# Kernel optimization log

Hardware: AMD Instinct MI355X
Metric: run time of the kernel (lower is better)

Reference implementation:

```python
import jax, jax.numpy as jnp
import numpy as np

N, E, CIN, COUT = 100000, 1600000, 64, 128
EPS = 1e-5  # torch BatchNorm default


def setup_inputs() -> dict:
    key = jax.random.key(0)
    ks = jax.random.split(key, 16)
    s = 0.1
    x = jax.random.normal(ks[0], (N, CIN), jnp.float32)
    src = jax.random.randint(ks[1], (E,), 0, N, dtype=jnp.int32)
    dst = jax.random.randint(ks[2], (E,), 0, N, dtype=jnp.int32)
    edge_index = jnp.stack([src, dst])  # [2, E]
    return {
        "x": x,
        "edge_index": edge_index,
        # conv0: GraphConv(CIN -> COUT)
        "W_root0": jax.random.normal(ks[3], (COUT, CIN), jnp.float32) * s,
        "W_nbr0": jax.random.normal(ks[4], (COUT, CIN), jnp.float32) * s,
        "b0": jnp.zeros((COUT,), jnp.float32),
        # bn0
        "g0": jnp.ones((COUT,), jnp.float32),
        "be0": jnp.zeros((COUT,), jnp.float32),
        # conv1: GraphConv(COUT -> COUT)
        "W_root1": jax.random.normal(ks[5], (COUT, COUT), jnp.float32) * s,
        "W_nbr1": jax.random.normal(ks[6], (COUT, COUT), jnp.float32) * s,
        "b1": jnp.zeros((COUT,), jnp.float32),
        # bn1
        "g1": jnp.ones((COUT,), jnp.float32),
        "be1": jnp.zeros((COUT,), jnp.float32),
        # residual 1x1 conv (Conv1d(CIN, COUT, 1))
        "Wlin": jax.random.normal(ks[7], (COUT, CIN), jnp.float32) * s,
        "blin": jnp.zeros((COUT,), jnp.float32),
    }


def graph_conv(x, src, dst, W_root, W_nbr, b):
    # PyG GraphConv: out_i = W_root x_i + W_nbr * sum_{j: (j->i) in E} x_j + b
    agg = jax.ops.segment_sum(x[src], dst, num_segments=N)  # scatter-add over edges
    return x @ W_root.T + agg @ W_nbr.T + b


def batch_norm(x, gamma, beta):
    # training-mode BatchNorm over the node dimension (biased variance)
    mu = jnp.mean(x, axis=0)
    var = jnp.mean(jnp.square(x - mu), axis=0)
    return (x - mu) * jax.lax.rsqrt(var + EPS) * gamma + beta


def reference(x, edge_index, W_root0, W_nbr0, b0, g0, be0,
              W_root1, W_nbr1, b1, g1, be1, Wlin, blin):
    src, dst = edge_index[0], edge_index[1]
    y = batch_norm(graph_conv(x, src, dst, W_root0, W_nbr0, b0), g0, be0)
    y = jax.nn.relu(y)
    y = batch_norm(graph_conv(y, src, dst, W_root1, W_nbr1, b1), g1, be1)
    out = y + (x @ Wlin.T + blin)  # 1x1 Conv1d residual projection
    return jax.nn.relu(out)
```

## Files before the change

### kernel.cpp

```cpp
#include <hip/hip_runtime.h>
#include <stdint.h>


#define CIN 64
#define COUT 128
#define BN_EPS 1e-5f
#define CURPAD 32
#define PCPAD 32
#define SPAD 32
#define PSH 8
#define PNODES (1 << PSH)
#define MAXP 512

typedef unsigned short u16;
typedef short short8 __attribute__((ext_vector_type(8)));
typedef float f32x4 __attribute__((ext_vector_type(4)));

__device__ __forceinline__ float bf2f(u16 u) {
    union { unsigned int i; float f; } v; v.i = ((unsigned int)u) << 16; return v.f;
}
__device__ __forceinline__ u16 f2bf(float f) {
    union { float f; unsigned int i; } v; v.f = f;
    unsigned int r = v.i + 0x7fffu + ((v.i >> 16) & 1u);
    return (u16)(r >> 16);
}
__device__ __forceinline__ float lo16(unsigned int w) { return bf2f((u16)(w & 0xffffu)); }
__device__ __forceinline__ float hi16(unsigned int w) { return bf2f((u16)(w >> 16)); }

template<bool BF> __device__ __forceinline__ float ldf(const void* p, long i) {
    if (BF) return bf2f(((const u16*)p)[i]);
    return ((const float*)p)[i];
}
template<bool BF> __device__ __forceinline__ short8 ld8(const void* p, long i) {
    if (BF) return *(const short8*)((const u16*)p + i);
    const float* f = (const float*)p + i;
    short8 r;
#pragma unroll
    for (int j = 0; j < 8; ++j) r[j] = (short)f2bf(f[j]);
    return r;
}

__global__ void k_detect(const unsigned int* __restrict__ x, int* __restrict__ flag) {
    int lane = threadIdx.x;
    int cnt = 0;
#pragma unroll
    for (int i = 0; i < 8; ++i) {
        unsigned int w = x[lane * 8 + i];
        unsigned int e0 = (w >> 7) & 0xFFu, e1 = (w >> 23) & 0xFFu;
        cnt += (e0 >= 0x60u && e0 <= 0x8Eu);
        cnt += (e1 >= 0x60u && e1 <= 0x8Eu);
    }
    for (int o = 32; o; o >>= 1) cnt += __shfl_down(cnt, o);
    if (lane == 0) *flag = (cnt > 850) ? 1 : 0;
}

__global__ __launch_bounds__(256) void k_phist(const int* __restrict__ dst,
                                               int* __restrict__ pcount, int E, int np) {
    __shared__ int h[MAXP];
    for (int i = threadIdx.x; i < np; i += 256) h[i] = 0;
    __syncthreads();
    int stride = gridDim.x * 256;
    for (int e = blockIdx.x * 256 + threadIdx.x; e < E; e += stride)
        atomicAdd(&h[dst[e] >> PSH], 1);
    __syncthreads();
    for (int i = threadIdx.x; i < np; i += 256)
        if (h[i]) atomicAdd(&pcount[i * PCPAD], h[i]);
}

__global__ void k_pscan(const int* __restrict__ pcount, int* __restrict__ pstart,
                        int* __restrict__ pcursor, int np, int E) {
    __shared__ int s[MAXP];
    int t = threadIdx.x;
    int v = (t < np) ? pcount[t * PCPAD] : 0;
    s[t] = v; __syncthreads();
    for (int o = 1; o < MAXP; o <<= 1) {
        int u = (t >= o) ? s[t - o] : 0;
        __syncthreads(); s[t] += u; __syncthreads();
    }
    if (t < np) {
        int ex = s[t] - v;
        pstart[t] = ex;
        pcursor[t * CURPAD] = ex;
    }
    if (t == 0) pstart[np] = E;
}

__global__ __launch_bounds__(256) void k_pfill(const int* __restrict__ src,
        const int* __restrict__ dst, int* __restrict__ pcursor,
        unsigned int* __restrict__ barr, int E, int np) {
    __shared__ int cnt[MAXP], gb[MAXP], loc[MAXP];
    int tid = threadIdx.x;
    int base = blockIdx.x * 4096;
    for (int i = tid; i < np; i += 256) { cnt[i] = 0; loc[i] = 0; }
    __syncthreads();
    int pk[16]; unsigned int rec[16];
#pragma unroll
    for (int k = 0; k < 16; ++k) {
        int e = base + k * 256 + tid;
        if (e < E) {
            int d = dst[e];
            pk[k] = d >> PSH;
            rec[k] = ((unsigned int)(d & (PNODES - 1)) << 20) | (unsigned int)src[e];
            atomicAdd(&cnt[pk[k]], 1);
        } else pk[k] = -1;
    }
    __syncthreads();
    for (int i = tid; i < np; i += 256)
        if (cnt[i]) gb[i] = atomicAdd(&pcursor[i * CURPAD], cnt[i]);
    __syncthreads();
#pragma unroll
    for (int k = 0; k < 16; ++k) {
        if (pk[k] >= 0) {
            int off = atomicAdd(&loc[pk[k]], 1);
            barr[gb[pk[k]] + off] = rec[k];
        }
    }
}

__global__ __launch_bounds__(256) void k_psort(const unsigned int* __restrict__ barr,
        const int* __restrict__ pstart, int* __restrict__ csr,
        int* __restrict__ row_start, int n, int np, int E) {
    __shared__ int hist[PNODES], curs[PNODES], tsum[256];
    int tid = threadIdx.x;
    int p = blockIdx.x;
    int e0 = pstart[p], e1 = pstart[p + 1];
    int node0 = p << PSH;
    hist[tid] = 0;
    __syncthreads();
    for (int t = e0 + tid; t < e1; t += 256)
        atomicAdd(&hist[barr[t] >> 20], 1);
    __syncthreads();
    int v = hist[tid];
    tsum[tid] = v; __syncthreads();
    for (int o = 1; o < 256; o <<= 1) {
        int u = (tid >= o) ? tsum[tid - o] : 0;
        __syncthreads(); tsum[tid] += u; __syncthreads();
    }
    int ex = tsum[tid] - v;
    curs[tid] = ex;
    int nd = node0 + tid;
    if (nd < n) row_start[nd] = e0 + ex;
    if (p == np - 1 && tid == 0) row_start[n] = E;
    __syncthreads();
    for (int t = e0 + tid; t < e1; t += 256) {
        unsigned int rec = barr[t];
        int pos = atomicAdd(&curs[rec >> 20], 1);
        csr[e0 + pos] = (int)(rec & 0xFFFFF);
    }
}

template<bool BF>
__device__ __forceinline__ void agg0_impl(const void* x, const int* rs, const int* csr,
                                          u16* agg, int n) {
    int i = blockIdx.x * 4 + (threadIdx.x >> 6);
    if (i >= n) return;
    int lane = threadIdx.x & 63;
    int slot = lane >> 4, cp = lane & 15;
    int b = rs[i], e = rs[i + 1];
    if (BF) {
        const unsigned int* x32 = (const unsigned int*)x;
        float acc[4] = {0.f, 0.f, 0.f, 0.f};
        int t = b + slot;
        for (; t + 12 < e; t += 16) {
            int j0 = csr[t], j1 = csr[t + 4], j2 = csr[t + 8], j3 = csr[t + 12];
            uint2 w0 = *((const uint2*)(x32 + (long)j0 * 32) + cp);
            uint2 w1 = *((const uint2*)(x32 + (long)j1 * 32) + cp);
            uint2 w2 = *((const uint2*)(x32 + (long)j2 * 32) + cp);
            uint2 w3 = *((const uint2*)(x32 + (long)j3 * 32) + cp);
            acc[0] += lo16(w0.x) + lo16(w1.x); acc[1] += hi16(w0.x) + hi16(w1.x);
            acc[2] += lo16(w0.y) + lo16(w1.y); acc[3] += hi16(w0.y) + hi16(w1.y);
            acc[0] += lo16(w2.x) + lo16(w3.x); acc[1] += hi16(w2.x) + hi16(w3.x);
            acc[2] += lo16(w2.y) + lo16(w3.y); acc[3] += hi16(w2.y) + hi16(w3.y);
        }
        for (; t < e; t += 4) {
            int j0 = csr[t];
            uint2 w0 = *((const uint2*)(x32 + (long)j0 * 32) + cp);
            acc[0] += lo16(w0.x); acc[1] += hi16(w0.x);
            acc[2] += lo16(w0.y); acc[3] += hi16(w0.y);
        }
#pragma unroll
        for (int k = 0; k < 4; ++k) {
            acc[k] += __shfl_xor(acc[k], 16);
            acc[k] += __shfl_xor(acc[k], 32);
        }
        if (slot == 0) {
            uint2 o;
            o.x = (unsigned int)f2bf(acc[0]) | ((unsigned int)f2bf(acc[1]) << 16);
            o.y = (unsigned int)f2bf(acc[2]) | ((unsigned int)f2bf(acc[3]) << 16);
            *((uint2*)((unsigned int*)agg + (long)i * 32) + cp) = o;
        }
    } else {
        float acc[4] = {0.f, 0.f, 0.f, 0.f};
        int t = b + slot;
        for (; t + 12 < e; t += 16) {
            int j0 = csr[t], j1 = csr[t + 4], j2 = csr[t + 8], j3 = csr[t + 12];
            float4 w0 = *((const float4*)((const float*)x + (long)j0 * 64) + cp);
            float4 w1 = *((const float4*)((const float*)x + (long)j1 * 64) + cp);
            float4 w2 = *((const float4*)((const float*)x + (long)j2 * 64) + cp);
            float4 w3 = *((const float4*)((const float*)x + (long)j3 * 64) + cp);
            acc[0] += (w0.x + w1.x) + (w2.x + w3.x);
            acc[1] += (w0.y + w1.y) + (w2.y + w3.y);
            acc[2] += (w0.z + w1.z) + (w2.z + w3.z);
            acc[3] += (w0.w + w1.w) + (w2.w + w3.w);
        }
        for (; t < e; t += 4) {
            int j0 = csr[t];
            float4 w0 = *((const float4*)((const float*)x + (long)j0 * 64) + cp);
            acc[0] += w0.x; acc[1] += w0.y; acc[2] += w0.z; acc[3] += w0.w;
        }
#pragma unroll
        for (int k = 0; k < 4; ++k) {
            acc[k] += __shfl_xor(acc[k], 16);
            acc[k] += __shfl_xor(acc[k], 32);
        }
        if (slot == 0) {
            uint2 o;
            o.x = (unsigned int)f2bf(acc[0]) | ((unsigned int)f2bf(acc[1]) << 16);
            o.y = (unsigned int)f2bf(acc[2]) | ((unsigned int)f2bf(acc[3]) << 16);
            *((uint2*)((unsigned int*)agg + (long)i * 32) + cp) = o;
        }
    }
}

__global__ __launch_bounds__(256) void k_agg0(const int* __restrict__ flag,
        const void* x, const int* __restrict__ rs, const int* __restrict__ csr,
        u16* __restrict__ agg, int n) {
    if (*flag) agg0_impl<true >(x, rs, csr, agg, n);
    else       agg0_impl<false>(x, rs, csr, agg, n);
}

__global__ __launch_bounds__(256) void k_y0p(unsigned int* __restrict__ y0,
        const float* __restrict__ sc, const float* __restrict__ sh, long nq) {
    long idx = (long)blockIdx.x * 256 + threadIdx.x;
    int colq = threadIdx.x & 15;
    float s8[8], h8[8];
#pragma unroll
    for (int j = 0; j < 8; ++j) { s8[j] = sc[colq * 8 + j]; h8[j] = sh[colq * 8 + j]; }
    long stride = (long)gridDim.x * 256;
    uint4* p = (uint4*)y0;
    for (; idx < nq; idx += stride) {
        uint4 w = p[idx];
        unsigned int r[4] = {w.x, w.y, w.z, w.w};
        uint4 o;
        unsigned int* po = (unsigned int*)&o;
#pragma unroll
        for (int d = 0; d < 4; ++d) {
            float a = fmaxf(lo16(r[d]) * s8[2 * d]     + h8[2 * d],     0.f);
            float b = fmaxf(hi16(r[d]) * s8[2 * d + 1] + h8[2 * d + 1], 0.f);
            po[d] = (unsigned int)f2bf(a) | ((unsigned int)f2bf(b) << 16);
        }
        p[idx] = o;
    }
}

__global__ __launch_bounds__(256) void k_agg1(const u16* __restrict__ y0p,
        const int* __restrict__ rs, const int* __restrict__ csr,
        u16* __restrict__ agg, int n) {
    int i = blockIdx.x * 4 + (threadIdx.x >> 6);
    if (i >= n) return;
    int lane = threadIdx.x & 63;
    int slot = lane >> 4, cp = lane & 15;
    const unsigned int* y32 = (const unsigned int*)y0p;
    int b = rs[i], e = rs[i + 1];
    float acc[8] = {0.f, 0.f, 0.f, 0.f, 0.f, 0.f, 0.f, 0.f};
    int t = b + slot;
    for (; t + 12 < e; t += 16) {
        int j0 = csr[t], j1 = csr[t + 4], j2 = csr[t + 8], j3 = csr[t + 12];
        uint4 w0 = *((const uint4*)(y32 + (long)j0 * 64) + cp);
        uint4 w1 = *((const uint4*)(y32 + (long)j1 * 64) + cp);
        uint4 w2 = *((const uint4*)(y32 + (long)j2 * 64) + cp);
        uint4 w3 = *((const uint4*)(y32 + (long)j3 * 64) + cp);
        acc[0] += lo16(w0.x) + lo16(w1.x); acc[1] += hi16(w0.x) + hi16(w1.x);
        acc[2] += lo16(w0.y) + lo16(w1.y); acc[3] += hi16(w0.y) + hi16(w1.y);
        acc[4] += lo16(w0.z) + lo16(w1.z); acc[5] += hi16(w0.z) + hi16(w1.z);
        acc[6] += lo16(w0.w) + lo16(w1.w); acc[7] += hi16(w0.w) + hi16(w1.w);
        acc[0] += lo16(w2.x) + lo16(w3.x); acc[1] += hi16(w2.x) + hi16(w3.x);
        acc[2] += lo16(w2.y) + lo16(w3.y); acc[3] += hi16(w2.y) + hi16(w3.y);
        acc[4] += lo16(w2.z) + lo16(w3.z); acc[5] += hi16(w2.z) + hi16(w3.z);
        acc[6] += lo16(w2.w) + lo16(w3.w); acc[7] += hi16(w2.w) + hi16(w3.w);
    }
    for (; t < e; t += 4) {
        int j0 = csr[t];
        uint4 w0 = *((const uint4*)(y32 + (long)j0 * 64) + cp);
        acc[0] += lo16(w0.x); acc[1] += hi16(w0.x);
        acc[2] += lo16(w0.y); acc[3] += hi16(w0.y);
        acc[4] += lo16(w0.z); acc[5] += hi16(w0.z);
        acc[6] += lo16(w0.w); acc[7] += hi16(w0.w);
    }
#pragma unroll
    for (int k = 0; k < 8; ++k) {
        acc[k] += __shfl_xor(acc[k], 16);
        acc[k] += __shfl_xor(acc[k], 32);
    }
    if (slot == 0) {
        uint4 o;
        o.x = (unsigned int)f2bf(acc[0]) | ((unsigned int)f2bf(acc[1]) << 16);
        o.y = (unsigned int)f2bf(acc[2]) | ((unsigned int)f2bf(acc[3]) << 16);
        o.z = (unsigned int)f2bf(acc[4]) | ((unsigned int)f2bf(acc[5]) << 16);
        o.w = (unsigned int)f2bf(acc[6]) | ((unsigned int)f2bf(acc[7]) << 16);
        *((uint4*)((unsigned int*)agg + (long)i * 64) + cp) = o;
    }
}

template<bool BF>
__device__ __forceinline__ void gemm0_impl(const void* x, const u16* agg,
                                           const void* Wr, const void* Wn,
                                           u16* y0, float* sumP, float* sqP,
                                           int n, int nch, u16* lds) {
    const int ST = 130;
    int tid = threadIdx.x;
    int wave = tid >> 6, lane = tid & 63, lr = lane & 15, q = lane >> 4;

    short8 wf[2][4];
#pragma unroll
    for (int i = 0; i < 2; ++i) {
        int c = (2 * wave + i) * 16 + lr;
#pragma unroll
        for (int ks = 0; ks < 4; ++ks) {
            const void* W = (ks < 2) ? Wr : Wn;
            wf[i][ks] = ld8<BF>(W, (long)c * CIN + (ks & 1) * 32 + q * 8);
        }
    }

    const int rowb = tid >> 3, wb = tid & 7;
    const int rowf = tid >> 4, wfc = tid & 15;
    short8 rbx[2]; float4 rfx[4]; short8 rag[2];

    auto regload = [&](long chunk0) {
        if (BF) {
#pragma unroll
            for (int i = 0; i < 2; ++i) {
                long rg = chunk0 + rowb + i * 32; if (rg > n - 1) rg = n - 1;
                rbx[i] = *(const short8*)((const u16*)x + rg * CIN + wb * 8);
            }
        } else {
#pragma unroll
            for (int i = 0; i < 4; ++i) {
                long rg = chunk0 + rowf + i * 16; if (rg > n - 1) rg = n - 1;
                rfx[i] = *(const float4*)((const float*)x + rg * CIN + wfc * 4);
            }
        }
#pragma unroll
        for (int i = 0; i < 2; ++i) {
            long rg = chunk0 + rowb + i * 32; if (rg > n - 1) rg = n - 1;
            rag[i] = *(const short8*)(agg + rg * CIN + wb * 8);
        }
    };

    float st[2] = {0.f, 0.f}, sq[2] = {0.f, 0.f};
    int ch = blockIdx.x;
    if (ch < nch) regload((long)ch * 64);
    for (; ch < nch; ch += gridDim.x) {
        long chunk0 = (long)ch * 64;
        __syncthreads();
        if (BF) {
#pragma unroll
            for (int i = 0; i < 2; ++i)
                *(short8*)(lds + (rowb + i * 32) * ST + wb * 8) = rbx[i];
        } else {
#pragma unroll
            for (int i = 0; i < 4; ++i) {
                u16* d = lds + (rowf + i * 16) * ST + wfc * 4;
                d[0] = f2bf(rfx[i].x); d[1] = f2bf(rfx[i].y);
                d[2] = f2bf(rfx[i].z); d[3] = f2bf(rfx[i].w);
            }
        }
#pragma unroll
        for (int i = 0; i < 2; ++i)
            *(short8*)(lds + (rowb + i * 32) * ST + 64 + wb * 8) = rag[i];
        __syncthreads();
        long nxt = (long)ch + gridDim.x;
        if (nxt < nch) regload(nxt * 64);

#pragma unroll
        for (int t = 0; t < 4; ++t) {
            short8 a[4];
#pragma unroll
            for (int ks = 0; ks < 4; ++ks)
                a[ks] = *(const short8*)(lds + (t * 16 + lr) * ST + ks * 32 + q * 8);
#pragma unroll
            for (int i = 0; i < 2; ++i) {
                f32x4 acc = {0.f, 0.f, 0.f, 0.f};
#pragma unroll
                for (int ks = 0; ks < 4; ++ks)
                    acc = __builtin_amdgcn_mfma_f32_16x16x32_bf16(a[ks], wf[i][ks], acc, 0, 0, 0);
                int c = (2 * wave + i) * 16 + lr;
#pragma unroll
                for (int r = 0; r < 4; ++r) {
                    long row = chunk0 + t * 16 + q * 4 + r;
                    if (row < n) {
                        y0[row * COUT + c] = f2bf(acc[r]);
                        st[i] += acc[r]; sq[i] += acc[r] * acc[r];
                    }
                }
            }
        }
    }
#pragma unroll
    for (int i = 0; i < 2; ++i) {
        st[i] += __shfl_xor(st[i], 16); st[i] += __shfl_xor(st[i], 32);
        sq[i] += __shfl_xor(sq[i], 16); sq[i] += __shfl_xor(sq[i], 32);
    }
    if (q == 0) {
#pragma unroll
        for (int i = 0; i < 2; ++i) {
            int c = (2 * wave + i) * 16 + lr;
            atomicAdd(&sumP[c * SPAD], st[i]);
            atomicAdd(&sqP[c * SPAD], sq[i]);
        }
    }
}

__global__ __launch_bounds__(256) void k_gemm0(const int* __restrict__ flag,
        const void* x, const u16* __restrict__ agg, const void* Wr, const void* Wn,
        u16* __restrict__ y0, float* __restrict__ sumP, float* __restrict__ sqP,
        int n, int nch) {
    __shared__ u16 lds[64 * 130];
    if (*flag) gemm0_impl<true >(x, agg, Wr, Wn, y0, sumP, sqP, n, nch, lds);
    else       gemm0_impl<false>(x, agg, Wr, Wn, y0, sumP, sqP, n, nch, lds);
}

template<bool BF>
__device__ __forceinline__ void gemm1_impl(const u16* y0p, const u16* agg,
                                           const void* Wr, const void* Wn,
                                           u16* y1, float* sumP, float* sqP,
                                           int n, int nch, u16* lds) {
    const int ST = 258;
    int tid = threadIdx.x;
    int wave = tid >> 6, lane = tid & 63, lr = lane & 15, q = lane >> 4;
    int c = wave * 16 + lr;

    short8 wf[8];
#pragma unroll
    for (int ks = 0; ks < 8; ++ks) {
        const void* W = (ks < 4) ? Wr : Wn;
        wf[ks] = ld8<BF>(W, (long)c * COUT + (ks & 3) * 32 + q * 8);
    }

    const int rowy = tid >> 4, wy = tid & 15;
    short8 ry[2], rag[2];
    auto regload = [&](long chunk0) {
#pragma unroll
        for (int i = 0; i < 2; ++i) {
            long rg = chunk0 + rowy + i * 32; if (rg > n - 1) rg = n - 1;
            ry[i]  = *(const short8*)(y0p + rg * COUT + wy * 8);
            rag[i] = *(const short8*)(agg + rg * COUT + wy * 8);
        }
    };

    float st = 0.f, sq = 0.f;
    int ch = blockIdx.x;
    if (ch < nch) regload((long)ch * 64);
    for (; ch < nch; ch += gridDim.x) {
        long chunk0 = (long)ch * 64;
        __syncthreads();
#pragma unroll
        for (int i = 0; i < 2; ++i) {
            *(short8*)(lds + (rowy + i * 32) * ST + wy * 8) = ry[i];
            *(short8*)(lds + (rowy + i * 32) * ST + 128 + wy * 8) = rag[i];
        }
        __syncthreads();
        long nxt = (long)ch + gridDim.x;
        if (nxt < nch) regload(nxt * 64);

#pragma unroll
        for (int t = 0; t < 4; ++t) {
            short8 a[8];
#pragma unroll
            for (int ks = 0; ks < 8; ++ks)
                a[ks] = *(const short8*)(lds + (t * 16 + lr) * ST + ks * 32 + q * 8);
            f32x4 acc = {0.f, 0.f, 0.f, 0.f};
#pragma unroll
            for (int ks = 0; ks < 8; ++ks)
                acc = __builtin_amdgcn_mfma_f32_16x16x32_bf16(a[ks], wf[ks], acc, 0, 0, 0);
#pragma unroll
            for (int r = 0; r < 4; ++r) {
                long row = chunk0 + t * 16 + q * 4 + r;
                if (row < n) {
                    y1[row * COUT + c] = f2bf(acc[r]);
                    st += acc[r]; sq += acc[r] * acc[r];
                }
            }
        }
    }
    st += __shfl_xor(st, 16); st += __shfl_xor(st, 32);
    sq += __shfl_xor(sq, 16); sq += __shfl_xor(sq, 32);
    if (q == 0) {
        atomicAdd(&sumP[c * SPAD], st);
        atomicAdd(&sqP[c * SPAD], sq);
    }
}

__global__ __launch_bounds__(512) void k_gemm1(const int* __restrict__ flag,
        const u16* __restrict__ y0p, const u16* __restrict__ agg,
        const void* Wr, const void* Wn,
        u16* y1_bf , u16* y1_ws,
        float* __restrict__ sumP, float* __restrict__ sqP, int n, int nch) {
    __shared__ u16 lds[64 * 258];
    u16* y1 = *flag ? y1_bf : y1_ws;
    if (*flag) gemm1_impl<true >(y0p, agg, Wr, Wn, y1, sumP, sqP, n, nch, lds);
    else       gemm1_impl<false>(y0p, agg, Wr, Wn, y1, sumP, sqP, n, nch, lds);
}

__global__ void k_bnfin(const int* __restrict__ flag,
                        const float* __restrict__ sumP, const float* __restrict__ sqP,
                        const void* g, const void* be,
                        float* __restrict__ scale, float* __restrict__ shift, int n) {
    int c = threadIdx.x;
    bool bf = (*flag != 0);
    float inv = 1.f / (float)n;
    float mu = sumP[c * SPAD] * inv;
    float var = fmaxf(sqP[c * SPAD] * inv - mu * mu, 0.f);
    float gv = bf ? bf2f(((const u16*)g)[c]) : ((const float*)g)[c];
    float bv = bf ? bf2f(((const u16*)be)[c]) : ((const float*)be)[c];
    float sc = gv * rsqrtf(var + BN_EPS);
    scale[c] = sc;
    shift[c] = bv - mu * sc;
}

template<bool BF>
__device__ __forceinline__ void final_impl(const void* x, const u16* y1,
                                           const void* Wlin, const void* blin,
                                           const float* sc, const float* sh,
                                           void* out, int n, int nch, u16* lds) {
    const int ST = 194;
    int tid = threadIdx.x;
    int wave = tid >> 6, lane = tid & 63, lr = lane & 15, q = lane >> 4;

    short8 wf[2][2];
    float blc[2], scc[2], shc[2];
#pragma unroll
    for (int i = 0; i < 2; ++i) {
        int c = (2 * wave + i) * 16 + lr;
#pragma unroll
        for (int ks = 0; ks < 2; ++ks)
            wf[i][ks] = ld8<BF>(Wlin, (long)c * CIN + ks * 32 + q * 8);
        blc[i] = ldf<BF>(blin, c);
        scc[i] = sc[c]; shc[i] = sh[c];
    }

    const int rowb = tid >> 3, wb = tid & 7;
    const int rowf = tid >> 4, wfc = tid & 15;
    const int rowy = tid >> 4, wy = tid & 15;
    short8 rbx[2]; float4 rfx[4]; short8 ry[4];

    auto regload = [&](long chunk0) {
        if (BF) {
#pragma unroll
            for (int i = 0; i < 2; ++i) {
                long rg = chunk0 + rowb + i * 32; if (rg > n - 1) rg = n - 1;
                rbx[i] = *(const short8*)((const u16*)x + rg * CIN + wb * 8);
            }
        } else {
#pragma unroll
            for (int i = 0; i < 4; ++i) {
                long rg = chunk0 + rowf + i * 16; if (rg > n - 1) rg = n - 1;
                rfx[i] = *(const float4*)((const float*)x + rg * CIN + wfc * 4);
            }
        }
#pragma unroll
        for (int i = 0; i < 4; ++i) {
            long rg = chunk0 + rowy + i * 16; if (rg > n - 1) rg = n - 1;
            ry[i] = *(const short8*)(y1 + rg * COUT + wy * 8);
        }
    };

    int ch = blockIdx.x;
    if (ch < nch) regload((long)ch * 64);
    for (; ch < nch; ch += gridDim.x) {
        long chunk0 = (long)ch * 64;
        __syncthreads();
        if (BF) {
#pragma unroll
            for (int i = 0; i < 2; ++i)
                *(short8*)(lds + (rowb + i * 32) * ST + wb * 8) = rbx[i];
        } else {
#pragma unroll
            for (int i = 0; i < 4; ++i) {
                u16* d = lds + (rowf + i * 16) * ST + wfc * 4;
                d[0] = f2bf(rfx[i].x); d[1] = f2bf(rfx[i].y);
                d[2] = f2bf(rfx[i].z); d[3] = f2bf(rfx[i].w);
            }
        }
#pragma unroll
        for (int i = 0; i < 4; ++i)
            *(short8*)(lds + (rowy + i * 16) * ST + 64 + wy * 8) = ry[i];
        __syncthreads();
        long nxt = (long)ch + gridDim.x;
        if (nxt < nch) regload(nxt * 64);

#pragma unroll
        for (int t = 0; t < 4; ++t) {
            short8 a[2];
#pragma unroll
            for (int ks = 0; ks < 2; ++ks)
                a[ks] = *(const short8*)(lds + (t * 16 + lr) * ST + ks * 32 + q * 8);
#pragma unroll
            for (int i = 0; i < 2; ++i) {
                f32x4 acc = {0.f, 0.f, 0.f, 0.f};
                acc = __builtin_amdgcn_mfma_f32_16x16x32_bf16(a[0], wf[i][0], acc, 0, 0, 0);
                acc = __builtin_amdgcn_mfma_f32_16x16x32_bf16(a[1], wf[i][1], acc, 0, 0, 0);
                int c = (2 * wave + i) * 16 + lr;
#pragma unroll
                for (int r = 0; r < 4; ++r) {
                    long row = chunk0 + t * 16 + q * 4 + r;
                    if (row < n) {
                        float yv = bf2f(lds[(t * 16 + q * 4 + r) * ST + 64 + c]);
                        float v = acc[r] + blc[i] + yv * scc[i] + shc[i];
                        v = fmaxf(v, 0.f);
                        if (BF) ((u16*)out)[row * COUT + c] = f2bf(v);
                        else    ((float*)out)[row * COUT + c] = v;
                    }
                }
            }
        }
    }
}

__global__ __launch_bounds__(256) void k_final(const int* __restrict__ flag,
        const void* x, const void* Wlin, const void* blin,
        const u16* y1_bf , const u16* y1_ws,
        const float* __restrict__ sc, const float* __restrict__ sh,
        void* out, int n, int nch) {
    __shared__ u16 lds[64 * 194];
    const u16* y1 = *flag ? y1_bf : y1_ws;
    if (*flag) final_impl<true >(x, y1, Wlin, blin, sc, sh, out, n, nch, lds);
    else       final_impl<false>(x, y1, Wlin, blin, sc, sh, out, n, nch, lds);
}

extern "C" void kernel_launch(void* const* d_in, const int* in_sizes, int n_in,
                              void* d_out, int out_size, void* d_ws, size_t ws_size,
                              hipStream_t stream) {
    (void)n_in; (void)out_size; (void)ws_size;
    const void* x    = d_in[0];
    const int*  ei   = (const int*)d_in[1];
    const void* Wr0  = d_in[2];
    const void* Wn0  = d_in[3];
    const void* g0   = d_in[5];
    const void* be0  = d_in[6];
    const void* Wr1  = d_in[7];
    const void* Wn1  = d_in[8];
    const void* g1   = d_in[10];
    const void* be1  = d_in[11];
    const void* Wlin = d_in[12];
    const void* blin = d_in[13];

    const int N = in_sizes[0] / CIN;
    const int E = in_sizes[1] / 2;
    const int* src = ei;
    const int* dst = ei + E;
    const int NP = (N + PNODES - 1) >> PSH;

    char* base = (char*)d_ws;
    size_t off = 0;
    auto carve = [&](size_t bytes) -> void* {
        void* p = base + off;
        off = (off + bytes + 255) & ~(size_t)255;
        return p;
    };
    int*   flag      = (int*)carve(256);
    int*   pcount    = (int*)carve(MAXP * PCPAD * sizeof(int));
    int*   pstart    = (int*)carve((MAXP + 1) * sizeof(int));
    int*   pcursor   = (int*)carve(MAXP * CURPAD * sizeof(int));
    float* statsP    = (float*)carve(4 * 128 * SPAD * sizeof(float));
    float* scsh      = (float*)carve(512 * sizeof(float));
    int*   row_start = (int*)carve((size_t)(N + 1) * sizeof(int));
    unsigned int* barr = (unsigned int*)carve((size_t)E * sizeof(int));
    int*   csr       = (int*)carve((size_t)E * sizeof(int));
    u16*   aggu      = (u16*)carve((size_t)N * COUT * sizeof(u16));
    u16*   y0        = (u16*)carve((size_t)N * COUT * sizeof(u16));
    u16*   y1_ws     = (u16*)carve((size_t)N * COUT * sizeof(u16));

    float* sum0P = statsP;
    float* sq0P  = statsP + 128 * SPAD;
    float* sum1P = statsP + 256 * SPAD;
    float* sq1P  = statsP + 384 * SPAD;

    hipMemsetAsync(pcount, 0, MAXP * PCPAD * sizeof(int), stream);
    hipMemsetAsync(statsP, 0, 4 * 128 * SPAD * sizeof(float), stream);

    const int nwb = (N + 3) / 4;
    const int nch = (N + 63) / 64;
    const int ntl = (E + 4095) / 4096;
    const int G   = nch < 1024 ? nch : 1024;
    const long nq = (long)N * 16;
    int g2 = (int)((nq + 255) / 256); if (g2 > 2048) g2 = 2048;

    k_detect<<<1, 64, 0, stream>>>((const unsigned int*)x, flag);

    k_phist<<<256, 256, 0, stream>>>(dst, pcount, E, NP);
    k_pscan<<<1, MAXP, 0, stream>>>(pcount, pstart, pcursor, NP, E);
    k_pfill<<<ntl, 256, 0, stream>>>(src, dst, pcursor, barr, E, NP);
    k_psort<<<NP, 256, 0, stream>>>(barr, pstart, csr, row_start, N, NP, E);

    k_agg0 <<<nwb, 256, 0, stream>>>(flag, x, row_start, csr, aggu, N);
    k_gemm0<<<G, 256, 0, stream>>>(flag, x, aggu, Wr0, Wn0, y0,
                                   sum0P, sq0P, N, nch);
    k_bnfin<<<1, 128, 0, stream>>>(flag, sum0P, sq0P, g0, be0,
                                   scsh, scsh + 128, N);

    k_y0p<<<g2, 256, 0, stream>>>((unsigned int*)y0, scsh, scsh + 128, nq);

    k_agg1 <<<nwb, 256, 0, stream>>>(y0, row_start, csr, aggu, N);
    k_gemm1<<<G, 512, 0, stream>>>(flag, y0, aggu, Wr1, Wn1,
                                   (u16*)d_out, y1_ws, sum1P, sq1P, N, nch);
    k_bnfin<<<1, 128, 0, stream>>>(flag, sum1P, sq1P, g1, be1,
                                   scsh + 256, scsh + 384, N);

    k_final<<<G, 256, 0, stream>>>(flag, x, Wlin, blin,
                                   (const u16*)d_out, y1_ws,
                                   scsh + 256, scsh + 384, d_out, N, nch);
}
```

Measured before the change: 401.8 us.

## Process two nodes per wave in agg1 and drop LDS staging in gemm1

k_agg1 now gives each wave two adjacent nodes and interleaves their neighbour gathers, so more independent memory loads are in flight per wave. k_gemm1 moves from 512 to 256 threads, with each wave computing two 16-column output tiles. It loads A fragments straight from global memory instead of staging them through LDS with a register prefetch and barriers. This removes the LDS traffic and syncs, but each A fragment load becomes a narrower strided global read and the explicit prefetch overlap is lost.

Result: no change. 402.6 us (+0.2%).

```diff
diff --git a/kernel.cpp b/kernel.cpp
--- a/kernel.cpp
+++ b/kernel.cpp
@@ -38,6 +38,13 @@
 #pragma unroll
     for (int j = 0; j < 8; ++j) r[j] = (short)f2bf(f[j]);
     return r;
+}
+
+__device__ __forceinline__ void acc8(float* a, uint4 w) {
+    a[0] += lo16(w.x); a[1] += hi16(w.x);
+    a[2] += lo16(w.y); a[3] += hi16(w.y);
+    a[4] += lo16(w.z); a[5] += hi16(w.z);
+    a[6] += lo16(w.w); a[7] += hi16(w.w);
 }
 
 __global__ void k_detect(const unsigned int* __restrict__ x, int* __restrict__ flag) {
@@ -256,49 +263,80 @@
 __global__ __launch_bounds__(256) void k_agg1(const u16* __restrict__ y0p,
         const int* __restrict__ rs, const int* __restrict__ csr,
         u16* __restrict__ agg, int n) {
-    int i = blockIdx.x * 4 + (threadIdx.x >> 6);
-    if (i >= n) return;
+    int i0 = blockIdx.x * 8 + ((threadIdx.x >> 6) << 1);
+    if (i0 >= n) return;
     int lane = threadIdx.x & 63;
     int slot = lane >> 4, cp = lane & 15;
     const unsigned int* y32 = (const unsigned int*)y0p;
-    int b = rs[i], e = rs[i + 1];
-    float acc[8] = {0.f, 0.f, 0.f, 0.f, 0.f, 0.f, 0.f, 0.f};
-    int t = b + slot;
-    for (; t + 12 < e; t += 16) {
-        int j0 = csr[t], j1 = csr[t + 4], j2 = csr[t + 8], j3 = csr[t + 12];
+    int i1 = i0 + 1;
+    int bA = rs[i0], eA = rs[i0 + 1];
+    int bB = eA, eB = (i1 < n) ? rs[i1 + 1] : eA;
+
+    float aA[8] = {0.f, 0.f, 0.f, 0.f, 0.f, 0.f, 0.f, 0.f};
+    float aB[8] = {0.f, 0.f, 0.f, 0.f, 0.f, 0.f, 0.f, 0.f};
+    int tA = bA + slot, tB = bB + slot;
+
+    while (tA + 12 < eA && tB + 12 < eB) {
+        int ja0 = csr[tA], ja1 = csr[tA + 4], ja2 = csr[tA + 8], ja3 = csr[tA + 12];
+        int jb0 = csr[tB], jb1 = csr[tB + 4], jb2 = csr[tB + 8], jb3 = csr[tB + 12];
+        uint4 wa0 = *((const uint4*)(y32 + (long)ja0 * 64) + cp);
+        uint4 wa1 = *((const uint4*)(y32 + (long)ja1 * 64) + cp);
+        uint4 wa2 = *((const uint4*)(y32 + (long)ja2 * 64) + cp);
+        uint4 wa3 = *((const uint4*)(y32 + (long)ja3 * 64) + cp);
+        uint4 wb0 = *((const uint4*)(y32 + (long)jb0 * 64) + cp);
+        uint4 wb1 = *((const uint4*)(y32 + (long)jb1 * 64) + cp);
+        uint4 wb2 = *((const uint4*)(y32 + (long)jb2 * 64) + cp);
+        uint4 wb3 = *((const uint4*)(y32 + (long)jb3 * 64) + cp);
+        acc8(aA, wa0); acc8(aA, wa1); acc8(aA, wa2); acc8(aA, wa3);
+        acc8(aB, wb0); acc8(aB, wb1); acc8(aB, wb2); acc8(aB, wb3);
+        tA += 16; tB += 16;
+    }
+    for (; tA + 12 < eA; tA += 16) {
+        int j0 = csr[tA], j1 = csr[tA + 4], j2 = csr[tA + 8], j3 = csr[tA + 12];
         uint4 w0 = *((const uint4*)(y32 + (long)j0 * 64) + cp);
         uint4 w1 = *((const uint4*)(y32 + (long)j1 * 64) + cp);
         uint4 w2 = *((const uint4*)(y32 + (long)j2 * 64) + cp);
         uint4 w3 = *((const uint4*)(y32 + (long)j3 * 64) + cp);
-        acc[0] += lo16(w0.x) + lo16(w1.x); acc[1] += hi16(w0.x) + hi16(w1.x);
-        acc[2] += lo16(w0.y) + lo16(w1.y); acc[3] += hi16(w0.y) + hi16(w1.y);
-        acc[4] += lo16(w0.z) + lo16(w1.z); acc[5] += hi16(w0.z) + hi16(w1.z);
-        acc[6] += lo16(w0.w) + lo16(w1.w); acc[7] += hi16(w0.w) + hi16(w1.w);
-        acc[0] += lo16(w2.x) + lo16(w3.x); acc[1] += hi16(w2.x) + hi16(w3.x);
-        acc[2] += lo16(w2.y) + lo16(w3.y); acc[3] += hi16(w2.y) + hi16(w3.y);
-        acc[4] += lo16(w2.z) + lo16(w3.z); acc[5] += hi16(w2.z) + hi16(w3.z);
-        acc[6] += lo16(w2.w) + lo16(w3.w); acc[7] += hi16(w2.w) + hi16(w3.w);
-    }
-    for (; t < e; t += 4) {
-        int j0 = csr[t];
+        acc8(aA, w0); acc8(aA, w1); acc8(aA, w2); acc8(aA, w3);
+    }
+    for (; tA < eA; tA += 4) {
+        uint4 w0 = *((const uint4*)(y32 + (long)csr[tA] * 64) + cp);
+        acc8(aA, w0);
+    }
+    for (; tB + 12 < eB; tB += 16) {
+        int j0 = csr[tB], j1 = csr[tB + 4], j2 = csr[tB + 8], j3 = csr[tB + 12];
         uint4 w0 = *((const uint4*)(y32 + (long)j0 * 64) + cp);
-        acc[0] += lo16(w0.x); acc[1] += hi16(w0.x);
-        acc[2] += lo16(w0.y); acc[3] += hi16(w0.y);
-        acc[4] += lo16(w0.z); acc[5] += hi16(w0.z);
-        acc[6] += lo16(w0.w); acc[7] += hi16(w0.w);
+        uint4 w1 = *((const uint4*)(y32 + (long)j1 * 64) + cp);
+        uint4 w2 = *((const uint4*)(y32 + (long)j2 * 64) + cp);
+        uint4 w3 = *((const uint4*)(y32 + (long)j3 * 64) + cp);
+        acc8(aB, w0); acc8(aB, w1); acc8(aB, w2); acc8(aB, w3);
+    }
+    for (; tB < eB; tB += 4) {
+        uint4 w0 = *((const uint4*)(y32 + (long)csr[tB] * 64) + cp);
+        acc8(aB, w0);
     }
 #pragma unroll
     for (int k = 0; k < 8; ++k) {
-        acc[k] += __shfl_xor(acc[k], 16);
-        acc[k] += __shfl_xor(acc[k], 32);
+        aA[k] += __shfl_xor(aA[k], 16);
+        aA[k] += __shfl_xor(aA[k], 32);
+        aB[k] += __shfl_xor(aB[k], 16);
+        aB[k] += __shfl_xor(aB[k], 32);
     }
     if (slot == 0) {
         uint4 o;
-        o.x = (unsigned int)f2bf(acc[0]) | ((unsigned int)f2bf(acc[1]) << 16);
-        o.y = (unsigned int)f2bf(acc[2]) | ((unsigned int)f2bf(acc[3]) << 16);
-        o.z = (unsigned int)f2bf(acc[4]) | ((unsigned int)f2bf(acc[5]) << 16);
-        o.w = (unsigned int)f2bf(acc[6]) | ((unsigned int)f2bf(acc[7]) << 16);
-        *((uint4*)((unsigned int*)agg + (long)i * 64) + cp) = o;
+        o.x = (unsigned int)f2bf(aA[0]) | ((unsigned int)f2bf(aA[1]) << 16);
+        o.y = (unsigned int)f2bf(aA[2]) | ((unsigned int)f2bf(aA[3]) << 16);
+        o.z = (unsigned int)f2bf(aA[4]) | ((unsigned int)f2bf(aA[5]) << 16);
+        o.w = (unsigned int)f2bf(aA[6]) | ((unsigned int)f2bf(aA[7]) << 16);
+        *((uint4*)((unsigned int*)agg + (long)i0 * 64) + cp) = o;
+        if (i1 < n) {
+            uint4 p;
+            p.x = (unsigned int)f2bf(aB[0]) | ((unsigned int)f2bf(aB[1]) << 16);
+            p.y = (unsigned int)f2bf(aB[2]) | ((unsigned int)f2bf(aB[3]) << 16);
+            p.z = (unsigned int)f2bf(aB[4]) | ((unsigned int)f2bf(aB[5]) << 16);
+            p.w = (unsigned int)f2bf(aB[6]) | ((unsigned int)f2bf(aB[7]) << 16);
+            *((uint4*)((unsigned int*)agg + (long)i1 * 64) + cp) = p;
+        }
     }
 }
 
@@ -424,82 +462,75 @@
 __device__ __forceinline__ void gemm1_impl(const u16* y0p, const u16* agg,
                                            const void* Wr, const void* Wn,
                                            u16* y1, float* sumP, float* sqP,
-                                           int n, int nch, u16* lds) {
-    const int ST = 258;
+                                           int n, int nch) {
     int tid = threadIdx.x;
     int wave = tid >> 6, lane = tid & 63, lr = lane & 15, q = lane >> 4;
-    int c = wave * 16 + lr;
-
-    short8 wf[8];
-#pragma unroll
-    for (int ks = 0; ks < 8; ++ks) {
-        const void* W = (ks < 4) ? Wr : Wn;
-        wf[ks] = ld8<BF>(W, (long)c * COUT + (ks & 3) * 32 + q * 8);
-    }
-
-    const int rowy = tid >> 4, wy = tid & 15;
-    short8 ry[2], rag[2];
-    auto regload = [&](long chunk0) {
+
+    short8 wf[2][8];
+#pragma unroll
+    for (int i = 0; i < 2; ++i) {
+        int c = (2 * wave + i) * 16 + lr;
+#pragma unroll
+        for (int ks = 0; ks < 8; ++ks) {
+            const void* W = (ks < 4) ? Wr : Wn;
+            wf[i][ks] = ld8<BF>(W, (long)c * COUT + (ks & 3) * 32 + q * 8);
+        }
+    }
+
+    float st[2] = {0.f, 0.f}, sq[2] = {0.f, 0.f};
+    for (int ch = blockIdx.x; ch < nch; ch += gridDim.x) {
+        long chunk0 = (long)ch * 64;
+#pragma unroll
+        for (int t = 0; t < 4; ++t) {
+            long rg = chunk0 + t * 16 + lr; if (rg > n - 1) rg = n - 1;
+            short8 a[8];
+#pragma unroll
+            for (int ks = 0; ks < 4; ++ks)
+                a[ks] = *(const short8*)(y0p + rg * COUT + ks * 32 + q * 8);
+#pragma unroll
+            for (int ks = 0; ks < 4; ++ks)
+                a[4 + ks] = *(const short8*)(agg + rg * COUT + ks * 32 + q * 8);
+#pragma unroll
+            for (int i = 0; i < 2; ++i) {
+                f32x4 acc = {0.f, 0.f, 0.f, 0.f};
+#pragma unroll
+                for (int ks = 0; ks < 8; ++ks)
+                    acc = __builtin_amdgcn_mfma_f32_16x16x32_bf16(a[ks], wf[i][ks], acc, 0, 0, 0);
+                int c = (2 * wave + i) * 16 + lr;
+#pragma unroll
+                for (int r = 0; r < 4; ++r) {
+                    long row = chunk0 + t * 16 + q * 4 + r;
+                    if (row < n) {
+                        y1[row * COUT + c] = f2bf(acc[r]);
+                        st[i] += acc[r]; sq[i] += acc[r] * acc[r];
+                    }
+                }
+            }
+        }
+    }
+#pragma unroll
+    for (int i = 0; i < 2; ++i) {
+        st[i] += __shfl_xor(st[i], 16); st[i] += __shfl_xor(st[i], 32);
+        sq[i] += __shfl_xor(sq[i], 16); sq[i] += __shfl_xor(sq[i], 32);
+    }
+    if (q == 0) {
 #pragma unroll
         for (int i = 0; i < 2; ++i) {
-            long rg = chunk0 + rowy + i * 32; if (rg > n - 1) rg = n - 1;
-            ry[i]  = *(const short8*)(y0p + rg * COUT + wy * 8);
-            rag[i] = *(const short8*)(agg + rg * COUT + wy * 8);
-        }
-    };
-
-    float st = 0.f, sq = 0.f;
-    int ch = blockIdx.x;
-    if (ch < nch) regload((long)ch * 64);
-    for (; ch < nch; ch += gridDim.x) {
-        long chunk0 = (long)ch * 64;
-        __syncthreads();
-#pragma unroll
-        for (int i = 0; i < 2; ++i) {
-            *(short8*)(lds + (rowy + i * 32) * ST + wy * 8) = ry[i];
-            *(short8*)(lds + (rowy + i * 32) * ST + 128 + wy * 8) = rag[i];
-        }
-        __syncthreads();
-        long nxt = (long)ch + gridDim.x;
-        if (nxt < nch) regload(nxt * 64);
-
-#pragma unroll
-        for (int t = 0; t < 4; ++t) {
-            short8 a[8];
-#pragma unroll
-            for (int ks = 0; ks < 8; ++ks)
-                a[ks] = *(const short8*)(lds + (t * 16 + lr) * ST + ks * 32 + q * 8);
-            f32x4 acc = {0.f, 0.f, 0.f, 0.f};
-#pragma unroll
-            for (int ks = 0; ks < 8; ++ks)
-                acc = __builtin_amdgcn_mfma_f32_16x16x32_bf16(a[ks], wf[ks], acc, 0, 0, 0);
-#pragma unroll
-            for (int r = 0; r < 4; ++r) {
-                long row = chunk0 + t * 16 + q * 4 + r;
-                if (row < n) {
-                    y1[row * COUT + c] = f2bf(acc[r]);
-                    st += acc[r]; sq += acc[r] * acc[r];
-                }
-            }
-        }
-    }
-    st += __shfl_xor(st, 16); st += __shfl_xor(st, 32);
-    sq += __shfl_xor(sq, 16); sq += __shfl_xor(sq, 32);
-    if (q == 0) {
-        atomicAdd(&sumP[c * SPAD], st);
-        atomicAdd(&sqP[c * SPAD], sq);
-    }
-}
-
-__global__ __launch_bounds__(512) void k_gemm1(const int* __restrict__ flag,
+            int c = (2 * wave + i) * 16 + lr;
+            atomicAdd(&sumP[c * SPAD], st[i]);
+            atomicAdd(&sqP[c * SPAD], sq[i]);
+        }
+    }
+}
+
+__global__ __launch_bounds__(256) void k_gemm1(const int* __restrict__ flag,
         const u16* __restrict__ y0p, const u16* __restrict__ agg,
         const void* Wr, const void* Wn,
         u16* y1_bf , u16* y1_ws,
         float* __restrict__ sumP, float* __restrict__ sqP, int n, int nch) {
-    __shared__ u16 lds[64 * 258];
     u16* y1 = *flag ? y1_bf : y1_ws;
-    if (*flag) gemm1_impl<true >(y0p, agg, Wr, Wn, y1, sumP, sqP, n, nch, lds);
-    else       gemm1_impl<false>(y0p, agg, Wr, Wn, y1, sumP, sqP, n, nch, lds);
+    if (*flag) gemm1_impl<true >(y0p, agg, Wr, Wn, y1, sumP, sqP, n, nch);
+    else       gemm1_impl<false>(y0p, agg, Wr, Wn, y1, sumP, sqP, n, nch);
 }
 
 __global__ void k_bnfin(const int* __restrict__ flag,
@@ -680,6 +711,7 @@
     hipMemsetAsync(statsP, 0, 4 * 128 * SPAD * sizeof(float), stream);
 
     const int nwb = (N + 3) / 4;
+    const int nwb2 = (N + 7) / 8;
     const int nch = (N + 63) / 64;
     const int ntl = (E + 4095) / 4096;
     const int G   = nch < 1024 ? nch : 1024;
@@ -701,8 +733,8 @@
 
     k_y0p<<<g2, 256, 0, stream>>>((unsigned int*)y0, scsh, scsh + 128, nq);
 
-    k_agg1 <<<nwb, 256, 0, stream>>>(y0, row_start, csr, aggu, N);
-    k_gemm1<<<G, 512, 0, stream>>>(flag, y0, aggu, Wr1, Wn1,
+    k_agg1 <<<nwb2, 256, 0, stream>>>(y0, row_start, csr, aggu, N);
+    k_gemm1<<<G, 256, 0, stream>>>(flag, y0, aggu, Wr1, Wn1,
                                    (u16*)d_out, y1_ws, sum1P, sq1P, N, nch);
     k_bnfin<<<1, 128, 0, stream>>>(flag, sum1P, sq1P, g1, be1,
                                    scsh + 256, scsh + 384, N);
```
